# Kernel optimization log

Hardware: AMD Instinct MI355X
Metric: run time of the kernel (lower is better)

Reference implementation:

```python
import jax, jax.numpy as jnp
import numpy as np


def _sq_cdist(a, b):
    # squared Euclidean distances, [N, M]
    a2 = jnp.sum(a * a, axis=1)[:, None]
    b2 = jnp.sum(b * b, axis=1)[None, :]
    d = a2 + b2 - 2.0 * (a @ b.T)
    return jnp.maximum(d, 0.0)


def _gaussian_kernel_mean(a, b, sigmas):
    # mean over N*M of sum_k exp(-dist / (2*sigma_k))
    dist = _sq_cdist(a, b)                      # [N, M]
    beta = 1.0 / (2.0 * sigmas)                 # [K]
    s = jnp.exp(-beta[:, None, None] * dist[None, :, :])  # [K, N, M]
    return jnp.mean(jnp.sum(s, axis=0))


def setup_inputs() -> dict:
    key = jax.random.key(0)
    k1, k2 = jax.random.split(key)
    B, C, H, W = 4, 256, 32, 32
    x = jax.random.normal(k1, (B, C, H, W), dtype=jnp.float32)
    y = jax.random.normal(k2, (B, C, H, W), dtype=jnp.float32)
    sigmas = jnp.array([0.01, 0.1, 1.0, 10.0, 100.0], dtype=jnp.float32)
    return {"x": x, "y": y, "sigmas": sigmas}


def reference(x, y, sigmas):
    B, C, H, W = x.shape
    # (B,C,H,W) -> (B*H*W, C), matching flatten(2).transpose(1,2).reshape(-1,C)
    xf = jnp.transpose(x.reshape(B, C, H * W), (0, 2, 1)).reshape(-1, C)
    yf = jnp.transpose(y.reshape(B, C, H * W), (0, 2, 1)).reshape(-1, C)
    xx = _gaussian_kernel_mean(xf, xf, sigmas)
    yy = _gaussian_kernel_mean(yf, yf, sigmas)
    xy = _gaussian_kernel_mean(xf, yf, sigmas)
    return xx + yy - 2.0 * xy
```

## Files before the change

### kernel.cpp

```cpp
#include <hip/hip_runtime.h>
#include <hip/hip_bf16.h>


#define NSIG 5
#define CKS   262144
#define NBLK2 2080

typedef __attribute__((ext_vector_type(8))) short short8;
typedef __attribute__((ext_vector_type(4))) float floatx4;

#define GLDS16(gp, lp) __builtin_amdgcn_global_load_lds( \
    (const __attribute__((address_space(1))) void*)(gp),  \
    (__attribute__((address_space(3))) void*)(lp), 16, 0, 0)

__global__ __launch_bounds__(256) void prep_kernel(const float* __restrict__ x,
                                                   const float* __restrict__ y,
                                                   ushort* __restrict__ Zc,
                                                   float* __restrict__ norms) {
    const int bid = blockIdx.x;
    const int t = threadIdx.x;
    const int s = bid >> 8;
    const int b = (bid >> 6) & 3;
    const int p0 = (bid & 63) << 4;
    const float* src = s ? y : x;
    const int n0 = (s << 12) + (b << 10) + p0;

    __shared__ float tile[256][17];

    const int cg = t >> 2;
    const int p4 = (t & 3) << 2;
#pragma unroll
    for (int pass = 0; pass < 4; ++pass) {
        const int c = cg + (pass << 6);
        const float4 v = *(const float4*)(src + (((size_t)((b << 8) + c)) << 10) + p0 + p4);
        tile[c][p4] = v.x; tile[c][p4 + 1] = v.y; tile[c][p4 + 2] = v.z; tile[c][p4 + 3] = v.w;
    }
    __syncthreads();

    const int r = t >> 4;
    const int q = t & 15;
    const int row = n0 + r;
    const int sw = (row >> 1) & 3;
    float nsum = 0.f;
#pragma unroll
    for (int h = 0; h < 2; ++h) {
        const int j = q + (h << 4);
        const int ck = j >> 2;
        const int sq = (j & 3) ^ sw;
        const int c0 = j << 3;
        uint pk[4];
#pragma unroll
        for (int jj = 0; jj < 4; ++jj) {
            const float f0 = tile[c0 + 2 * jj][r];
            const float f1 = tile[c0 + 2 * jj + 1][r];
            const __hip_bfloat16 h0 = __float2bfloat16(f0);
            const __hip_bfloat16 h1 = __float2bfloat16(f1);
            const float q0 = __bfloat162float(h0), q1 = __bfloat162float(h1);
            nsum = fmaf(q0, q0, nsum);
            nsum = fmaf(q1, q1, nsum);
            pk[jj] = (uint)(*(const ushort*)&h0) | ((uint)(*(const ushort*)&h1) << 16);
        }
        *(uint4*)(Zc + (size_t)ck * CKS + (size_t)row * 32 + (sq << 3)) =
            make_uint4(pk[0], pk[1], pk[2], pk[3]);
    }
#pragma unroll
    for (int off = 1; off < 16; off <<= 1) nsum += __shfl_xor(nsum, off, 32);
    if (q == 0) norms[row] = nsum;
}

__global__ __launch_bounds__(256) void gemm_epi(const ushort* __restrict__ Zc,
                                                const float* __restrict__ norms,
                                                const float* __restrict__ sigmas,
                                                float* __restrict__ partials) {
    __shared__ ushort bufA[3][4096];
    __shared__ ushort bufB[3][4096];
    __shared__ float wsum[4];

    const int t = threadIdx.x;
    const int w = t >> 6, l = t & 63;
    const int m = l & 15, q = l >> 4;

    const int lin = blockIdx.x;
    int p = (int)((-4.0f + sqrtf(16.0f + 128.0f * (float)lin)) * (1.0f / 64.0f));
    p = p < 0 ? 0 : (p > 7 ? 7 : p);
    while (p < 7 && 32 * (p + 1) * (p + 1) + 4 * (p + 1) <= lin) ++p;
    while (p > 0 && 32 * p * p + 4 * p > lin) --p;
    const int o = lin - (32 * p * p + 4 * p);
    int c = 7;
#pragma unroll
    for (int cc = 7; cc >= 1; --cc) {
        const int Q = cc * (8 * p + 1) + (cc * (cc - 1)) / 2;
        if (o < Q) c = cc - 1;
    }
    const int Qc = c * (8 * p + 1) + (c * (c - 1)) / 2;
    const int tj2 = 8 * p + c;
    const int ti2 = o - Qc;

    const int I0 = ti2 << 7;
    const int J0 = tj2 << 7;

    const int ti = (ti2 << 1) + (w >> 1);
    const int tj = (tj2 << 1) + (w & 1);
    const bool active = (ti <= tj);
    const bool diag = (ti == tj);
    const int i0 = ti << 6, j0 = tj << 6;

    int loffA[4], loffB[4];
#pragma unroll
    for (int f = 0; f < 4; ++f) {
        const int ra = ((w >> 1) << 6) + (f << 4) + m;
        loffA[f] = (ra << 5) + ((q ^ ((ra >> 1) & 3)) << 3);
        const int rb = ((w & 1) << 6) + (f << 4) + m;
        loffB[f] = (rb << 5) + ((q ^ ((rb >> 1) & 3)) << 3);
    }

    const int sg = (w << 10) + (l << 3);
    const ushort* gA0 = Zc + (size_t)I0 * 32 + sg;
    const ushort* gB0 = Zc + (size_t)J0 * 32 + sg;
    const int lo = w << 10;

    GLDS16(gA0,        &bufA[0][lo]);
    GLDS16(gA0 + 512,  &bufA[0][lo + 512]);
    GLDS16(gB0,        &bufB[0][lo]);
    GLDS16(gB0 + 512,  &bufB[0][lo + 512]);
    GLDS16(gA0 + CKS,       &bufA[1][lo]);
    GLDS16(gA0 + CKS + 512, &bufA[1][lo + 512]);
    GLDS16(gB0 + CKS,       &bufB[1][lo]);
    GLDS16(gB0 + CKS + 512, &bufB[1][lo + 512]);
    asm volatile("s_waitcnt vmcnt(4)" ::: "memory");
    __builtin_amdgcn_s_barrier();
    __builtin_amdgcn_sched_barrier(0);

    floatx4 accf[4][4];
#pragma unroll
    for (int fi = 0; fi < 4; ++fi)
#pragma unroll
        for (int fj = 0; fj < 4; ++fj) accf[fi][fj] = (floatx4){0.f, 0.f, 0.f, 0.f};

#pragma unroll
    for (int ck = 0; ck < 8; ++ck) {
        const ushort* rA = &bufA[ck % 3][0];
        const ushort* rB = &bufB[ck % 3][0];
        short8 fa[4], fb[4];
#pragma unroll
        for (int f = 0; f < 4; ++f) fa[f] = *(const short8*)(rA + loffA[f]);
#pragma unroll
        for (int f = 0; f < 4; ++f) fb[f] = *(const short8*)(rB + loffB[f]);
        if (ck < 6) {
            const size_t ko = (size_t)(ck + 2) * CKS;
            const int nb = (ck + 2) % 3;
            GLDS16(gA0 + ko,       &bufA[nb][lo]);
            GLDS16(gA0 + ko + 512, &bufA[nb][lo + 512]);
            GLDS16(gB0 + ko,       &bufB[nb][lo]);
            GLDS16(gB0 + ko + 512, &bufB[nb][lo + 512]);
        }
#pragma unroll
        for (int fi = 0; fi < 4; ++fi)
#pragma unroll
            for (int fj = 0; fj < 4; ++fj)
                accf[fi][fj] = __builtin_amdgcn_mfma_f32_16x16x32_bf16(fa[fi], fb[fj], accf[fi][fj], 0, 0, 0);
        if (ck < 7) {
            if (ck < 6) { asm volatile("s_waitcnt vmcnt(4)" ::: "memory"); }
            else        { asm volatile("s_waitcnt vmcnt(0)" ::: "memory"); }
            __builtin_amdgcn_s_barrier();
            __builtin_amdgcn_sched_barrier(0);
        }
    }

    float lsum = 0.f;
    if (active) {
        float c2[NSIG];
#pragma unroll
        for (int k = 0; k < NSIG; ++k) c2[k] = (-0.5f / sigmas[k]) * 1.44269504f;

        const float sgn2 = ((i0 < 4096) == (j0 < 4096)) ? 2.f : -2.f;

        float njs[4];
#pragma unroll
        for (int fj = 0; fj < 4; ++fj) njs[fj] = norms[j0 + (fj << 4) + m];

#pragma unroll
        for (int fi = 0; fi < 4; ++fi) {
            const floatx4 ni4 = *(const floatx4*)(norms + i0 + (fi << 4) + (q << 2));
#pragma unroll
            for (int fj = 0; fj < 4; ++fj) {
                floatx4 a = accf[fi][fj];
#pragma unroll
                for (int v = 0; v < 4; ++v)
                    a[v] = fmaxf(fmaf(-2.f, a[v], ni4[v] + njs[fj]), 0.f);
                accf[fi][fj] = a;
            }
        }
        if (diag) {
#pragma unroll
            for (int fi = 0; fi < 4; ++fi)
#pragma unroll
                for (int fj = 0; fj < 4; ++fj)
#pragma unroll
                    for (int v = 0; v < 4; ++v) {
                        const int dif = ((fi - fj) << 4) + ((q << 2) + v) - m;
                        if (dif >= 0) accf[fi][fj][v] = 3.0e9f;
                    }
        }

        floatx4 mn = accf[0][0];
#pragma unroll
        for (int fi = 0; fi < 4; ++fi)
#pragma unroll
            for (int fj = 0; fj < 4; ++fj)
                if (fi | fj) {
#pragma unroll
                    for (int v = 0; v < 4; ++v) mn[v] = fminf(mn[v], accf[fi][fj][v]);
                }
        float dmin = fminf(fminf(mn[0], mn[1]), fminf(mn[2], mn[3]));
#pragma unroll
        for (int off = 1; off < 64; off <<= 1) dmin = fminf(dmin, __shfl_xor(dmin, off, 64));

        floatx4 ts0 = (floatx4){0.f, 0.f, 0.f, 0.f};
        floatx4 ts1 = (floatx4){0.f, 0.f, 0.f, 0.f};
#pragma unroll
        for (int k = 0; k < NSIG; ++k) {
            if (c2[k] * dmin >= -126.f) {
                const float ck2 = c2[k];
#pragma unroll
                for (int fi = 0; fi < 4; ++fi)
#pragma unroll
                    for (int fj = 0; fj < 4; ++fj) {
                        const floatx4 a = accf[fi][fj];
                        floatx4 e;
#pragma unroll
                        for (int v = 0; v < 4; ++v)
                            e[v] = __builtin_amdgcn_exp2f(ck2 * a[v]);
                        if ((fj & 1) == 0) ts0 += e; else ts1 += e;
                    }
            }
        }
        ts0 += ts1;
        lsum = sgn2 * ((ts0[0] + ts0[1]) + (ts0[2] + ts0[3]));
    }

#pragma unroll
    for (int off = 32; off > 0; off >>= 1) lsum += __shfl_down(lsum, off, 64);
    if (l == 0) wsum[w] = lsum;
    __syncthreads();
    if (t == 0) partials[blockIdx.x] = wsum[0] + wsum[1] + wsum[2] + wsum[3];
}

__global__ __launch_bounds__(256) void finalize_kernel(const float* __restrict__ partials,
                                                       float* __restrict__ out) {
    __shared__ double sh[256];
    const int t = threadIdx.x;
    double s = 0.0;
    for (int i = t; i < NBLK2; i += 256) s += (double)partials[i];
    sh[t] = s;
    __syncthreads();
    for (int st = 128; st > 0; st >>= 1) {
        if (t < st) sh[t] += sh[t + st];
        __syncthreads();
    }
    if (t == 0) out[0] = (float)((sh[0] + 8192.0 * NSIG) * (1.0 / (4096.0 * 4096.0)));
}

extern "C" void kernel_launch(void* const* d_in, const int* in_sizes, int n_in,
                              void* d_out, int out_size, void* d_ws, size_t ws_size,
                              hipStream_t stream) {
    const float* x   = (const float*)d_in[0];
    const float* y   = (const float*)d_in[1];
    const float* sig = (const float*)d_in[2];

    ushort* Zc      = (ushort*)d_ws;
    float* norms    = (float*)((char*)d_ws + (size_t)8192 * 256 * 2);
    float* partials = (float*)((char*)norms + 8192 * sizeof(float));
    float* out      = (float*)d_out;

    prep_kernel<<<512, 256, 0, stream>>>(x, y, Zc, norms);
    gemm_epi<<<NBLK2, 256, 0, stream>>>(Zc, norms, sig, partials);
    finalize_kernel<<<1, 256, 0, stream>>>(partials, out);
}
```

Measured before the change: 95.99 us.

## Restructure GEMM K-loop into double-buffered 64-wide stages with fewer barriers

The K loop is rebuilt from a 3-slot ring of 32-wide chunks (8 iterations, one barrier each) into a 2-stage double buffer where each stage holds two 32-wide chunks (4 iterations). The aim is to halve the barrier and waitcnt synchronisation count and give each iteration more MFMA work. The trade-off is that the next stage's loads are issued only after a full vmcnt(0) wait and barrier, so prefetch distance shrinks and load latency may be exposed. LDS use also grows from 3 to 4 chunk slots per operand.

```diff
diff --git a/kernel.cpp b/kernel.cpp
--- a/kernel.cpp
+++ b/kernel.cpp
@@ -72,8 +72,8 @@
                                                 const float* __restrict__ norms,
                                                 const float* __restrict__ sigmas,
                                                 float* __restrict__ partials) {
-    __shared__ ushort bufA[3][4096];
-    __shared__ ushort bufB[3][4096];
+    __shared__ ushort bufA[2][2][4096];
+    __shared__ ushort bufB[2][2][4096];
     __shared__ float wsum[4];
 
     const int t = threadIdx.x;
@@ -119,15 +119,22 @@
     const ushort* gB0 = Zc + (size_t)J0 * 32 + sg;
     const int lo = w << 10;
 
-    GLDS16(gA0,        &bufA[0][lo]);
-    GLDS16(gA0 + 512,  &bufA[0][lo + 512]);
-    GLDS16(gB0,        &bufB[0][lo]);
-    GLDS16(gB0 + 512,  &bufB[0][lo + 512]);
-    GLDS16(gA0 + CKS,       &bufA[1][lo]);
-    GLDS16(gA0 + CKS + 512, &bufA[1][lo + 512]);
-    GLDS16(gB0 + CKS,       &bufB[1][lo]);
-    GLDS16(gB0 + CKS + 512, &bufB[1][lo + 512]);
-    asm volatile("s_waitcnt vmcnt(4)" ::: "memory");
+#define STAGE64(c_, s_) do {                                              \
+        const size_t k0_ = (size_t)(2 * (c_)) * CKS;                      \
+        const size_t k1_ = (size_t)(2 * (c_) + 1) * CKS;                  \
+        GLDS16(gA0 + k0_,       &bufA[s_][0][lo]);                        \
+        GLDS16(gA0 + k0_ + 512, &bufA[s_][0][lo + 512]);                  \
+        GLDS16(gA0 + k1_,       &bufA[s_][1][lo]);                        \
+        GLDS16(gA0 + k1_ + 512, &bufA[s_][1][lo + 512]);                  \
+        GLDS16(gB0 + k0_,       &bufB[s_][0][lo]);                        \
+        GLDS16(gB0 + k0_ + 512, &bufB[s_][0][lo + 512]);                  \
+        GLDS16(gB0 + k1_,       &bufB[s_][1][lo]);                        \
+        GLDS16(gB0 + k1_ + 512, &bufB[s_][1][lo + 512]);                  \
+    } while (0)
+
+    STAGE64(0, 0);
+    STAGE64(1, 1);
+    asm volatile("s_waitcnt vmcnt(8)" ::: "memory");
     __builtin_amdgcn_s_barrier();
     __builtin_amdgcn_sched_barrier(0);
 
@@ -138,34 +145,33 @@
         for (int fj = 0; fj < 4; ++fj) accf[fi][fj] = (floatx4){0.f, 0.f, 0.f, 0.f};
 
 #pragma unroll
-    for (int ck = 0; ck < 8; ++ck) {
-        const ushort* rA = &bufA[ck % 3][0];
-        const ushort* rB = &bufB[ck % 3][0];
-        short8 fa[4], fb[4];
-#pragma unroll
-        for (int f = 0; f < 4; ++f) fa[f] = *(const short8*)(rA + loffA[f]);
-#pragma unroll
-        for (int f = 0; f < 4; ++f) fb[f] = *(const short8*)(rB + loffB[f]);
-        if (ck < 6) {
-            const size_t ko = (size_t)(ck + 2) * CKS;
-            const int nb = (ck + 2) % 3;
-            GLDS16(gA0 + ko,       &bufA[nb][lo]);
-            GLDS16(gA0 + ko + 512, &bufA[nb][lo + 512]);
-            GLDS16(gB0 + ko,       &bufB[nb][lo]);
-            GLDS16(gB0 + ko + 512, &bufB[nb][lo + 512]);
-        }
-#pragma unroll
-        for (int fi = 0; fi < 4; ++fi)
-#pragma unroll
-            for (int fj = 0; fj < 4; ++fj)
-                accf[fi][fj] = __builtin_amdgcn_mfma_f32_16x16x32_bf16(fa[fi], fb[fj], accf[fi][fj], 0, 0, 0);
-        if (ck < 7) {
-            if (ck < 6) { asm volatile("s_waitcnt vmcnt(4)" ::: "memory"); }
-            else        { asm volatile("s_waitcnt vmcnt(0)" ::: "memory"); }
+    for (int ck = 0; ck < 4; ++ck) {
+        const int sl = ck & 1;
+        short8 fa[2][4], fb[2][4];
+#pragma unroll
+        for (int s = 0; s < 2; ++s) {
+#pragma unroll
+            for (int f = 0; f < 4; ++f) {
+                fa[s][f] = *(const short8*)(&bufA[sl][s][0] + loffA[f]);
+                fb[s][f] = *(const short8*)(&bufB[sl][s][0] + loffB[f]);
+            }
+        }
+#pragma unroll
+        for (int s = 0; s < 2; ++s)
+#pragma unroll
+            for (int fi = 0; fi < 4; ++fi)
+#pragma unroll
+                for (int fj = 0; fj < 4; ++fj)
+                    accf[fi][fj] = __builtin_amdgcn_mfma_f32_16x16x32_bf16(
+                        fa[s][fi], fb[s][fj], accf[fi][fj], 0, 0, 0);
+        if (ck < 3) {
+            asm volatile("s_waitcnt vmcnt(0)" ::: "memory");
             __builtin_amdgcn_s_barrier();
             __builtin_amdgcn_sched_barrier(0);
-        }
-    }
+            if (ck < 2) STAGE64(ck + 2, sl);
+        }
+    }
+#undef STAGE64
 
     float lsum = 0.f;
     if (active) {
```

New measurement: 102.5 us. +6.8%, slower.

## Split 128x128 gemm tile across 8 waves with 32x64 per-wave subtiles

Applied to the files above, without the earlier changes.

Raises the gemm block from 4 to 8 waves, so each wave computes a 32x64 subtile instead of 64x64. Each thread now issues half as many global-to-LDS loads, holds half the accumulators, and does half the exp work in the epilogue. Diagonal-tile masking and skipping are reworked at the finer granularity, and the whole lower-triangle wave pairs on diagonal supertiles are disabled. This is meant to raise occupancy and latency hiding on the exp-heavy epilogue. The cost is more LDS fragment reads per MFMA, since A reuse per B fragment drops.

```diff
diff --git a/kernel.cpp b/kernel.cpp
--- a/kernel.cpp
+++ b/kernel.cpp
@@ -68,13 +68,13 @@
     if (q == 0) norms[row] = nsum;
 }
 
-__global__ __launch_bounds__(256) void gemm_epi(const ushort* __restrict__ Zc,
+__global__ __launch_bounds__(512) void gemm_epi(const ushort* __restrict__ Zc,
                                                 const float* __restrict__ norms,
                                                 const float* __restrict__ sigmas,
                                                 float* __restrict__ partials) {
     __shared__ ushort bufA[3][4096];
     __shared__ ushort bufB[3][4096];
-    __shared__ float wsum[4];
+    __shared__ float wsum[8];
 
     const int t = threadIdx.x;
     const int w = t >> 6, l = t & 63;
@@ -95,45 +95,45 @@
     const int Qc = c * (8 * p + 1) + (c * (c - 1)) / 2;
     const int tj2 = 8 * p + c;
     const int ti2 = o - Qc;
+    const bool diagST = (ti2 == tj2);
 
     const int I0 = ti2 << 7;
     const int J0 = tj2 << 7;
 
-    const int ti = (ti2 << 1) + (w >> 1);
-    const int tj = (tj2 << 1) + (w & 1);
-    const bool active = (ti <= tj);
-    const bool diag = (ti == tj);
-    const int i0 = ti << 6, j0 = tj << 6;
-
-    int loffA[4], loffB[4];
+    const int rs = w >> 1;
+    const int cs = w & 1;
+    const bool active = !(diagST && cs == 0 && rs >= 2);
+    const int i0 = I0 + (rs << 5);
+    const int j0 = J0 + (cs << 6);
+
+    int loffA[2], loffB[4];
+#pragma unroll
+    for (int f = 0; f < 2; ++f) {
+        const int ra = (rs << 5) + (f << 4) + m;
+        loffA[f] = (ra << 5) + ((q ^ ((ra >> 1) & 3)) << 3);
+    }
 #pragma unroll
     for (int f = 0; f < 4; ++f) {
-        const int ra = ((w >> 1) << 6) + (f << 4) + m;
-        loffA[f] = (ra << 5) + ((q ^ ((ra >> 1) & 3)) << 3);
-        const int rb = ((w & 1) << 6) + (f << 4) + m;
+        const int rb = (cs << 6) + (f << 4) + m;
         loffB[f] = (rb << 5) + ((q ^ ((rb >> 1) & 3)) << 3);
     }
 
-    const int sg = (w << 10) + (l << 3);
+    const int sg = (w << 9) + (l << 3);
     const ushort* gA0 = Zc + (size_t)I0 * 32 + sg;
     const ushort* gB0 = Zc + (size_t)J0 * 32 + sg;
-    const int lo = w << 10;
-
-    GLDS16(gA0,        &bufA[0][lo]);
-    GLDS16(gA0 + 512,  &bufA[0][lo + 512]);
-    GLDS16(gB0,        &bufB[0][lo]);
-    GLDS16(gB0 + 512,  &bufB[0][lo + 512]);
-    GLDS16(gA0 + CKS,       &bufA[1][lo]);
-    GLDS16(gA0 + CKS + 512, &bufA[1][lo + 512]);
-    GLDS16(gB0 + CKS,       &bufB[1][lo]);
-    GLDS16(gB0 + CKS + 512, &bufB[1][lo + 512]);
-    asm volatile("s_waitcnt vmcnt(4)" ::: "memory");
+    const int lo = w << 9;
+
+    GLDS16(gA0,       &bufA[0][lo]);
+    GLDS16(gB0,       &bufB[0][lo]);
+    GLDS16(gA0 + CKS, &bufA[1][lo]);
+    GLDS16(gB0 + CKS, &bufB[1][lo]);
+    asm volatile("s_waitcnt vmcnt(2)" ::: "memory");
     __builtin_amdgcn_s_barrier();
     __builtin_amdgcn_sched_barrier(0);
 
-    floatx4 accf[4][4];
-#pragma unroll
-    for (int fi = 0; fi < 4; ++fi)
+    floatx4 accf[2][4];
+#pragma unroll
+    for (int fi = 0; fi < 2; ++fi)
 #pragma unroll
         for (int fj = 0; fj < 4; ++fj) accf[fi][fj] = (floatx4){0.f, 0.f, 0.f, 0.f};
 
@@ -141,26 +141,24 @@
     for (int ck = 0; ck < 8; ++ck) {
         const ushort* rA = &bufA[ck % 3][0];
         const ushort* rB = &bufB[ck % 3][0];
-        short8 fa[4], fb[4];
-#pragma unroll
-        for (int f = 0; f < 4; ++f) fa[f] = *(const short8*)(rA + loffA[f]);
+        short8 fa[2], fb[4];
+#pragma unroll
+        for (int f = 0; f < 2; ++f) fa[f] = *(const short8*)(rA + loffA[f]);
 #pragma unroll
         for (int f = 0; f < 4; ++f) fb[f] = *(const short8*)(rB + loffB[f]);
         if (ck < 6) {
             const size_t ko = (size_t)(ck + 2) * CKS;
             const int nb = (ck + 2) % 3;
-            GLDS16(gA0 + ko,       &bufA[nb][lo]);
-            GLDS16(gA0 + ko + 512, &bufA[nb][lo + 512]);
-            GLDS16(gB0 + ko,       &bufB[nb][lo]);
-            GLDS16(gB0 + ko + 512, &bufB[nb][lo + 512]);
-        }
-#pragma unroll
-        for (int fi = 0; fi < 4; ++fi)
+            GLDS16(gA0 + ko, &bufA[nb][lo]);
+            GLDS16(gB0 + ko, &bufB[nb][lo]);
+        }
+#pragma unroll
+        for (int fi = 0; fi < 2; ++fi)
 #pragma unroll
             for (int fj = 0; fj < 4; ++fj)
                 accf[fi][fj] = __builtin_amdgcn_mfma_f32_16x16x32_bf16(fa[fi], fb[fj], accf[fi][fj], 0, 0, 0);
         if (ck < 7) {
-            if (ck < 6) { asm volatile("s_waitcnt vmcnt(4)" ::: "memory"); }
+            if (ck < 6) { asm volatile("s_waitcnt vmcnt(2)" ::: "memory"); }
             else        { asm volatile("s_waitcnt vmcnt(0)" ::: "memory"); }
             __builtin_amdgcn_s_barrier();
             __builtin_amdgcn_sched_barrier(0);
@@ -180,7 +178,7 @@
         for (int fj = 0; fj < 4; ++fj) njs[fj] = norms[j0 + (fj << 4) + m];
 
 #pragma unroll
-        for (int fi = 0; fi < 4; ++fi) {
+        for (int fi = 0; fi < 2; ++fi) {
             const floatx4 ni4 = *(const floatx4*)(norms + i0 + (fi << 4) + (q << 2));
 #pragma unroll
             for (int fj = 0; fj < 4; ++fj) {
@@ -191,21 +189,22 @@
                 accf[fi][fj] = a;
             }
         }
-        if (diag) {
-#pragma unroll
-            for (int fi = 0; fi < 4; ++fi)
+        if (diagST) {
+#pragma unroll
+            for (int fi = 0; fi < 2; ++fi)
 #pragma unroll
                 for (int fj = 0; fj < 4; ++fj)
 #pragma unroll
                     for (int v = 0; v < 4; ++v) {
-                        const int dif = ((fi - fj) << 4) + ((q << 2) + v) - m;
+                        const int dif = (rs << 5) + (fi << 4) + (q << 2) + v
+                                      - (cs << 6) - (fj << 4) - m;
                         if (dif >= 0) accf[fi][fj][v] = 3.0e9f;
                     }
         }
 
         floatx4 mn = accf[0][0];
 #pragma unroll
-        for (int fi = 0; fi < 4; ++fi)
+        for (int fi = 0; fi < 2; ++fi)
 #pragma unroll
             for (int fj = 0; fj < 4; ++fj)
                 if (fi | fj) {
@@ -223,7 +222,7 @@
             if (c2[k] * dmin >= -126.f) {
                 const float ck2 = c2[k];
 #pragma unroll
-                for (int fi = 0; fi < 4; ++fi)
+                for (int fi = 0; fi < 2; ++fi)
 #pragma unroll
                     for (int fj = 0; fj < 4; ++fj) {
                         const floatx4 a = accf[fi][fj];
@@ -243,7 +242,12 @@
     for (int off = 32; off > 0; off >>= 1) lsum += __shfl_down(lsum, off, 64);
     if (l == 0) wsum[w] = lsum;
     __syncthreads();
-    if (t == 0) partials[blockIdx.x] = wsum[0] + wsum[1] + wsum[2] + wsum[3];
+    if (t == 0) {
+        float s = 0.f;
+#pragma unroll
+        for (int i = 0; i < 8; ++i) s += wsum[i];
+        partials[blockIdx.x] = s;
+    }
 }
 
 __global__ __launch_bounds__(256) void finalize_kernel(const float* __restrict__ partials,
@@ -274,6 +278,6 @@
     float* out      = (float*)d_out;
 
     prep_kernel<<<512, 256, 0, stream>>>(x, y, Zc, norms);
-    gemm_epi<<<NBLK2, 256, 0, stream>>>(Zc, norms, sig, partials);
+    gemm_epi<<<NBLK2, 512, 0, stream>>>(Zc, norms, sig, partials);
     finalize_kernel<<<1, 256, 0, stream>>>(partials, out);
 }
```

Result: slower. 99.87 us (+4.0%).
